# Kernel tuning notes

Hardware: AMD Instinct MI355X
Metric: run time of the kernel (lower is better)

The kernel has to match this reference:

```python
import jax, jax.numpy as jnp
import numpy as np

N_NODES = 50000
N_EDGES = 800000
IN_DIM = 128
E_FEATS = 64
H = 8
D = IN_DIM // H
NEG_SLOPE = 0.2


def setup_inputs() -> dict:
    key = jax.random.key(0)
    ks = jax.random.split(key, 9)
    h = jax.random.normal(ks[0], (N_NODES, IN_DIM), dtype=jnp.float32)
    edge_features = jax.random.normal(ks[1], (N_EDGES, E_FEATS), dtype=jnp.float32)
    src = jax.random.randint(ks[2], (N_EDGES,), 0, N_NODES, dtype=jnp.int32)
    dst = jax.random.randint(ks[3], (N_EDGES,), 0, N_NODES, dtype=jnp.int32)
    s = 0.05
    Wq = jax.random.normal(ks[4], (IN_DIM, IN_DIM), dtype=jnp.float32) * s
    Wk = jax.random.normal(ks[5], (IN_DIM, IN_DIM), dtype=jnp.float32) * s
    Wv = jax.random.normal(ks[6], (IN_DIM, IN_DIM), dtype=jnp.float32) * s
    We = jax.random.normal(ks[7], (H, E_FEATS), dtype=jnp.float32) * s
    Wres = jax.random.normal(ks[8], (IN_DIM, IN_DIM), dtype=jnp.float32) * s
    return {"h": h, "edge_features": edge_features, "src": src, "dst": dst,
            "Wq": Wq, "Wk": Wk, "Wv": Wv, "We": We, "Wres": Wres}


def reference(h, edge_features, src, dst, Wq, Wk, Wv, We, Wres):
    N = h.shape[0]
    # QKV projections (feat_drop is identity at eval)
    q = (h @ Wq.T).reshape(N, H, D)
    k = (h @ Wk.T).reshape(N, H, D)
    v = (h @ Wv.T).reshape(N, H, D)
    # ee / m_att are computed in the original forward but never used (dead code)
    _ee = edge_features @ We.T  # [E, H]

    # v_dot_u('q','k'): dot(q[dst], k[src]) per edge, per head -> [E, H]
    e = jnp.einsum('ehd,ehd->eh', q[dst], k[src])
    e = jnp.where(e >= 0, e, NEG_SLOPE * e)  # leaky_relu

    # edge_softmax over incoming edges of each destination node
    m = jax.ops.segment_max(e, dst, num_segments=N)          # [N, H]
    ex = jnp.exp(e - m[dst])                                 # [E, H]
    z = jax.ops.segment_sum(ex, dst, num_segments=N)         # [N, H]
    alpha = ex / z[dst]                                      # [E, H] (attn_drop identity)

    # weighted aggregation: sum_e alpha * v[src]
    msg = v[src] * alpha[:, :, None]                         # [E, H, D]
    rst = jax.ops.segment_sum(msg, dst, num_segments=N)      # [N, H, D]
    rst = rst.reshape(N, H * D)
    rst = rst + h @ Wres.T                                   # residual
    return rst
```

## Files before the change

### kernel.cpp

```cpp
#include <hip/hip_runtime.h>


#define NEG_SLOPE 0.2f
#define CB 1024

typedef __attribute__((ext_vector_type(8))) short short8;
typedef __attribute__((ext_vector_type(4))) float f32x4;

__device__ __forceinline__ unsigned short f2bf(float f) {
    unsigned int u = __builtin_bit_cast(unsigned int, f);
    u = (u + 0x7fffu + ((u >> 16) & 1u)) >> 16;
    return (unsigned short)u;
}
__device__ __forceinline__ float bf2f(unsigned short s) {
    unsigned int u = (unsigned int)s << 16;
    return __builtin_bit_cast(float, u);
}

__global__ __launch_bounds__(256) void zero_wconv_kernel(
    const float* __restrict__ Wq, const float* __restrict__ Wk,
    const float* __restrict__ Wv, const float* __restrict__ Wres,
    unsigned short* __restrict__ wpk, int* __restrict__ cnt,
    int* __restrict__ csr_pad, int n4)
{
    int t = blockIdx.x * 256 + threadIdx.x;
    if (t < 8192) {
        int l = t & 63;
        int v = t >> 6;
        int kk = v & 3;
        int wct = v >> 2;
        int ct = wct & 7;
        int w = wct >> 3;
        const float* W = (w == 0) ? Wq : (w == 1) ? Wk : (w == 2) ? Wv : Wres;
        const float* srcp = W + (size_t)(ct * 16 + (l & 15)) * 128 + kk * 32 + (l >> 4) * 8;
        float4 lo = *reinterpret_cast<const float4*>(srcp);
        float4 hi = *reinterpret_cast<const float4*>(srcp + 4);
        short8 o;
        o[0] = (short)f2bf(lo.x); o[1] = (short)f2bf(lo.y);
        o[2] = (short)f2bf(lo.z); o[3] = (short)f2bf(lo.w);
        o[4] = (short)f2bf(hi.x); o[5] = (short)f2bf(hi.y);
        o[6] = (short)f2bf(hi.z); o[7] = (short)f2bf(hi.w);
        *reinterpret_cast<short8*>(wpk + (size_t)t * 8) = o;
        if (t < 64) csr_pad[t] = 0;
    } else {
        int u = t - 8192;
        if (u < n4) reinterpret_cast<int4*>(cnt)[u] = make_int4(0, 0, 0, 0);
    }
}

__global__ __launch_bounds__(256) void proj_count_kernel(
    const float* __restrict__ h,
    const unsigned short* __restrict__ wpk,
    unsigned short* __restrict__ qb, unsigned char* __restrict__ kvb,
    float* __restrict__ kvscl, unsigned short* __restrict__ resb,
    const int* __restrict__ dst, int* __restrict__ cnt,
    int N, int E, int PB)
{
    if (blockIdx.x >= PB) {
        int start = (blockIdx.x - PB) * 256 + threadIdx.x;
        for (int e = start; e < E; e += CB * 256)
            atomicAdd(&cnt[dst[e]], 1);
        return;
    }

    const int wid = threadIdx.x >> 6;
    const int lane = threadIdx.x & 63;
    const int row0 = blockIdx.x * 128 + wid * 32;
    const int r = lane & 15, g = lane >> 4;

    short8 afrag[2][4];
    #pragma unroll
    for (int grp = 0; grp < 2; ++grp) {
        int arow = row0 + grp * 16 + r;
        if (arow >= N) arow = N - 1;
        const float* hrow = h + (size_t)arow * 128 + g * 8;
        #pragma unroll
        for (int kk = 0; kk < 4; ++kk) {
            float4 lo = *reinterpret_cast<const float4*>(hrow + kk * 32);
            float4 hi = *reinterpret_cast<const float4*>(hrow + kk * 32 + 4);
            short8 a;
            a[0] = (short)f2bf(lo.x); a[1] = (short)f2bf(lo.y);
            a[2] = (short)f2bf(lo.z); a[3] = (short)f2bf(lo.w);
            a[4] = (short)f2bf(hi.x); a[5] = (short)f2bf(hi.y);
            a[6] = (short)f2bf(hi.z); a[7] = (short)f2bf(hi.w);
            afrag[grp][kk] = a;
        }
    }

    #pragma unroll
    for (int sec = 0; sec < 2; ++sec) {
        const int w = (sec == 0) ? 0 : 3;
        unsigned short* O = (sec == 0) ? qb : resb;
        #pragma unroll
        for (int ct = 0; ct < 8; ++ct) {
            const unsigned short* bp =
                wpk + ((size_t)((w * 8 + ct) * 4) * 64 + lane) * 8;
            f32x4 acc[2];
            acc[0] = (f32x4)(0.f); acc[1] = (f32x4)(0.f);
            #pragma unroll
            for (int kk = 0; kk < 4; ++kk) {
                short8 bfrag = *reinterpret_cast<const short8*>(bp + (size_t)kk * 512);
                acc[0] = __builtin_amdgcn_mfma_f32_16x16x32_bf16(
                    afrag[0][kk], bfrag, acc[0], 0, 0, 0);
                acc[1] = __builtin_amdgcn_mfma_f32_16x16x32_bf16(
                    afrag[1][kk], bfrag, acc[1], 0, 0, 0);
            }
            #pragma unroll
            for (int grp = 0; grp < 2; ++grp)
                #pragma unroll
                for (int j = 0; j < 4; ++j) {
                    int orow = row0 + grp * 16 + g * 4 + j;
                    if (orow < N)
                        O[(size_t)orow * 128 + ct * 16 + r] = f2bf(acc[grp][j]);
                }
        }
    }

    #pragma unroll
    for (int sec = 0; sec < 2; ++sec) {
        const int w = 1 + sec;
        f32x4 av[2][8];
        #pragma unroll
        for (int grp = 0; grp < 2; ++grp)
            #pragma unroll
            for (int ct = 0; ct < 8; ++ct) av[grp][ct] = (f32x4)(0.f);

        #pragma unroll
        for (int ct = 0; ct < 8; ++ct) {
            const unsigned short* bp =
                wpk + ((size_t)((w * 8 + ct) * 4) * 64 + lane) * 8;
            #pragma unroll
            for (int kk = 0; kk < 4; ++kk) {
                short8 bfrag = *reinterpret_cast<const short8*>(bp + (size_t)kk * 512);
                av[0][ct] = __builtin_amdgcn_mfma_f32_16x16x32_bf16(
                    afrag[0][kk], bfrag, av[0][ct], 0, 0, 0);
                av[1][ct] = __builtin_amdgcn_mfma_f32_16x16x32_bf16(
                    afrag[1][kk], bfrag, av[1][ct], 0, 0, 0);
            }
        }

        #pragma unroll
        for (int grp = 0; grp < 2; ++grp)
            #pragma unroll
            for (int j = 0; j < 4; ++j) {
                int orow = row0 + grp * 16 + g * 4 + j;
                float m = fabsf(av[grp][0][j]);
                #pragma unroll
                for (int ct = 1; ct < 8; ++ct)
                    m = fmaxf(m, fabsf(av[grp][ct][j]));
                #pragma unroll
                for (int s = 1; s < 16; s <<= 1)
                    m = fmaxf(m, __shfl_xor(m, s, 64));
                float scale = m * (1.f / 127.f);
                float inv = (m > 0.f) ? 127.f / m : 0.f;
                if (orow < N) {
                    #pragma unroll
                    for (int ct = 0; ct < 8; ++ct) {
                        int qv = (int)rintf(av[grp][ct][j] * inv);
                        kvb[(size_t)orow * 256 + 32 * ct + 8 * (r >> 2)
                            + (r & 3) + sec * 4] = (unsigned char)(signed char)qv;
                    }
                    if (r == 0) kvscl[2 * orow + sec] = scale;
                }
            }
    }
}

__global__ __launch_bounds__(256) void blocksum_kernel(
    const int* __restrict__ cnt, int* __restrict__ bsum, int N)
{
    __shared__ int ws[4];
    const int tid = threadIdx.x;
    int base = blockIdx.x * 1024 + tid * 4;
    int s = 0;
    if (base + 3 < N) {
        int4 v = *reinterpret_cast<const int4*>(cnt + base);
        s = v.x + v.y + v.z + v.w;
    } else {
        for (int i = 0; i < 4; ++i)
            if (base + i < N) s += cnt[base + i];
    }
    #pragma unroll
    for (int m = 32; m >= 1; m >>= 1) s += __shfl_xor(s, m, 64);
    if ((tid & 63) == 0) ws[tid >> 6] = s;
    __syncthreads();
    if (tid == 0) bsum[blockIdx.x] = ws[0] + ws[1] + ws[2] + ws[3];
}

__global__ __launch_bounds__(256) void scanfinal_kernel(
    const int* __restrict__ cnt, const int* __restrict__ bsum,
    int* __restrict__ row_start, int* __restrict__ cursor,
    int N, int E, int NB)
{
    __shared__ int sboff;
    __shared__ int wsum[4];
    const int tid = threadIdx.x, lane = tid & 63, w = tid >> 6;

    if (tid < 64) {
        int v = (tid < NB && tid < blockIdx.x) ? bsum[tid] : 0;
        #pragma unroll
        for (int m = 32; m >= 1; m >>= 1) v += __shfl_xor(v, m, 64);
        if (tid == 0) sboff = v;
    }
    __syncthreads();

    int base = blockIdx.x * 1024 + tid * 4;
    int a0 = 0, a1 = 0, a2 = 0, a3 = 0;
    if (base + 3 < N) {
        int4 v = *reinterpret_cast<const int4*>(cnt + base);
        a0 = v.x; a1 = v.y; a2 = v.z; a3 = v.w;
    } else {
        if (base + 0 < N) a0 = cnt[base + 0];
        if (base + 1 < N) a1 = cnt[base + 1];
        if (base + 2 < N) a2 = cnt[base + 2];
        if (base + 3 < N) a3 = cnt[base + 3];
    }
    const int tsum = a0 + a1 + a2 + a3;
    int v = tsum;
    #pragma unroll
    for (int off = 1; off < 64; off <<= 1) {
        int t = __shfl_up(v, off, 64);
        if (lane >= off) v += t;
    }
    if (lane == 63) wsum[w] = v;
    __syncthreads();
    int woff = 0;
    for (int i = 0; i < w; ++i) woff += wsum[i];
    int run = sboff + woff + v - tsum;

    int r0 = run, r1 = run + a0, r2 = r1 + a1, r3 = r2 + a2;
    if (base + 3 < N) {
        int4 o = make_int4(r0, r1, r2, r3);
        *reinterpret_cast<int4*>(row_start + base) = o;
        *reinterpret_cast<int4*>(cursor + base) = o;
    } else {
        int rr[4] = {r0, r1, r2, r3};
        for (int i = 0; i < 4; ++i)
            if (base + i < N) { row_start[base + i] = rr[i]; cursor[base + i] = rr[i]; }
    }
    if (blockIdx.x == 0 && tid == 0) row_start[N] = E;
}

__global__ __launch_bounds__(256) void scatter_kernel(
    const int* __restrict__ src, const int* __restrict__ dst,
    int* __restrict__ cursor, int* __restrict__ csr_src, int E)
{
    int e = blockIdx.x * 256 + threadIdx.x;
    if (e < E) {
        int d = dst[e];
        int pos = atomicAdd(&cursor[d], 1);
        csr_src[pos] = src[e];
    }
}

__global__ __launch_bounds__(256) void fused_agg_kernel(
    const unsigned short* __restrict__ qb,
    const unsigned char* __restrict__ kvb,
    const float2* __restrict__ kvscl,
    const unsigned short* __restrict__ resb,
    const int* __restrict__ row_start, const int* __restrict__ csr_src,
    float* __restrict__ rst, int N)
{
    const int lane = threadIdx.x & 63;
    const int j = lane & 31;
    const int half = lane >> 5;
    const int node = blockIdx.x * 4 + (threadIdx.x >> 6);
    if (node >= N) return;

    const int beg = row_start[node];
    const int nE  = row_start[node + 1] - beg;
    const int* cp = csr_src + beg;

    ushort4 qraw = *reinterpret_cast<const ushort4*>(qb + (size_t)node * 128 + 4 * j);
    const float q0 = bf2f(qraw.x), q1 = bf2f(qraw.y),
                q2 = bf2f(qraw.z), q3 = bf2f(qraw.w);

    float zA = 0.f, zB = 0.f;
    float aA0 = 0.f, aA1 = 0.f, aA2 = 0.f, aA3 = 0.f;
    float aB0 = 0.f, aB1 = 0.f, aB2 = 0.f, aB3 = 0.f;

    if (nE > 0) {
        int sa = cp[half];
        int sb = cp[half + 2];

        for (int i = 0; i < nE; i += 4) {
            const int ii = i + half;
            const float m0 = (ii < nE) ? 1.f : 0.f;
            const float m1 = (ii + 2 < nE) ? 1.f : 0.f;
            const int s0 = sa, s1 = sb;
            sa = cp[ii + 4];
            sb = cp[ii + 6];

            uint2 kv0 = *reinterpret_cast<const uint2*>(kvb + (size_t)s0 * 256 + 8 * j);
            uint2 kv1 = *reinterpret_cast<const uint2*>(kvb + (size_t)s1 * 256 + 8 * j);
            float2 sc0 = kvscl[s0];
            float2 sc1 = kvscl[s1];

            float p0 = q0 * (float)(signed char)(kv0.x)
                     + q1 * (float)(signed char)(kv0.x >> 8)
                     + q2 * (float)(signed char)(kv0.x >> 16)
                     + q3 * (float)(signed char)(kv0.x >> 24);
            float p1 = q0 * (float)(signed char)(kv1.x)
                     + q1 * (float)(signed char)(kv1.x >> 8)
                     + q2 * (float)(signed char)(kv1.x >> 16)
                     + q3 * (float)(signed char)(kv1.x >> 24);
            p0 += __shfl_xor(p0, 1, 64);
            p0 += __shfl_xor(p0, 2, 64);
            p1 += __shfl_xor(p1, 1, 64);
            p1 += __shfl_xor(p1, 2, 64);
            p0 *= sc0.x;
            p1 *= sc1.x;
            float e0 = (p0 >= 0.f) ? p0 : NEG_SLOPE * p0;
            float e1 = (p1 >= 0.f) ? p1 : NEG_SLOPE * p1;
            e0 = m0 * __expf(e0);
            e1 = m1 * __expf(e1);
            zA += e0;
            zB += e1;
            const float f0 = e0 * sc0.y;
            const float f1 = e1 * sc1.y;
            aA0 = fmaf(f0, (float)(signed char)(kv0.y),       aA0);
            aA1 = fmaf(f0, (float)(signed char)(kv0.y >> 8),  aA1);
            aA2 = fmaf(f0, (float)(signed char)(kv0.y >> 16), aA2);
            aA3 = fmaf(f0, (float)(signed char)(kv0.y >> 24), aA3);
            aB0 = fmaf(f1, (float)(signed char)(kv1.y),       aB0);
            aB1 = fmaf(f1, (float)(signed char)(kv1.y >> 8),  aB1);
            aB2 = fmaf(f1, (float)(signed char)(kv1.y >> 16), aB2);
            aB3 = fmaf(f1, (float)(signed char)(kv1.y >> 24), aB3);
        }
    }

    float a0 = aA0 + aB0, a1 = aA1 + aB1, a2 = aA2 + aB2, a3 = aA3 + aB3;
    float z = zA + zB;
    a0 += __shfl_xor(a0, 32, 64);
    a1 += __shfl_xor(a1, 32, 64);
    a2 += __shfl_xor(a2, 32, 64);
    a3 += __shfl_xor(a3, 32, 64);
    z  += __shfl_xor(z, 32, 64);

    if (half == 0) {
        const size_t base = (size_t)node * 128 + 4 * j;
        ushort4 rb = *reinterpret_cast<const ushort4*>(resb + base);
        float inv = (nE > 0) ? 1.f / z : 0.f;
        float4 rv;
        rv.x = fmaf(a0, inv, bf2f(rb.x));
        rv.y = fmaf(a1, inv, bf2f(rb.y));
        rv.z = fmaf(a2, inv, bf2f(rb.z));
        rv.w = fmaf(a3, inv, bf2f(rb.w));
        *reinterpret_cast<float4*>(rst + base) = rv;
    }
}

extern "C" void kernel_launch(void* const* d_in, const int* in_sizes, int n_in,
                              void* d_out, int out_size, void* d_ws, size_t ws_size,
                              hipStream_t stream) {
    const float* h    = (const float*)d_in[0];
    const int*   src  = (const int*)d_in[2];
    const int*   dst  = (const int*)d_in[3];
    const float* Wq   = (const float*)d_in[4];
    const float* Wk   = (const float*)d_in[5];
    const float* Wv   = (const float*)d_in[6];
    const float* Wres = (const float*)d_in[8];
    float* rst = (float*)d_out;

    const int N = in_sizes[0] / 128;
    const int E = in_sizes[2];

    unsigned short* qb   = (unsigned short*)d_ws;
    unsigned short* resb = qb + (size_t)N * 128;
    unsigned char*  kvb  = (unsigned char*)(resb + (size_t)N * 128);
    float*          kvscl = (float*)(kvb + (size_t)N * 256);
    unsigned short* wpk  = (unsigned short*)(kvscl + 2 * N);
    int* cnt       = (int*)(wpk + 4 * 16384);
    int* row_start = cnt + N;
    int* cursor    = row_start + (N + 1);
    int* csr_src   = cursor + N;
    int* bsum      = csr_src + E + 64;

    const int n4 = N / 4;
    const int NB = (N + 1023) / 1024;
    const int PB = (N + 127) / 128;

    zero_wconv_kernel<<<(8192 + n4 + 255) / 256, 256, 0, stream>>>(
        Wq, Wk, Wv, Wres, wpk, cnt, csr_src + E, n4);
    proj_count_kernel<<<PB + CB, 256, 0, stream>>>(
        h, wpk, qb, kvb, kvscl, resb, dst, cnt, N, E, PB);
    blocksum_kernel<<<NB, 256, 0, stream>>>(cnt, bsum, N);
    scanfinal_kernel<<<NB, 256, 0, stream>>>(cnt, bsum, row_start, cursor,
                                             N, E, NB);
    scatter_kernel<<<(E + 255) / 256, 256, 0, stream>>>(src, dst, cursor,
                                                        csr_src, E);
    fused_agg_kernel<<<(N + 3) / 4, 256, 0, stream>>>(
        qb, kvb, (const float2*)kvscl, resb, row_start, csr_src, rst, N);
}
```

Baseline: 159.0 us.

## Recompute K/V projections in two passes and store scales as bf16

The K/V quantization stops keeping all 16 accumulator tiles live. It runs the MFMAs once to compute per-row abs max, then recomputes them to quantize, which reduces register pressure at the cost of doubled K/V matmul work. The per-node dequantization scales are stored as packed bf16 pairs, halving the scale gather in the aggregation kernel. This costs slightly lower scale precision.

```diff
diff --git a/kernel.cpp b/kernel.cpp
--- a/kernel.cpp
+++ b/kernel.cpp
@@ -52,7 +52,7 @@
     const float* __restrict__ h,
     const unsigned short* __restrict__ wpk,
     unsigned short* __restrict__ qb, unsigned char* __restrict__ kvb,
-    float* __restrict__ kvscl, unsigned short* __restrict__ resb,
+    unsigned short* __restrict__ kvscl16, unsigned short* __restrict__ resb,
     const int* __restrict__ dst, int* __restrict__ cnt,
     int N, int E, int PB)
 {
@@ -119,50 +119,75 @@
     #pragma unroll
     for (int sec = 0; sec < 2; ++sec) {
         const int w = 1 + sec;
-        f32x4 av[2][8];
+
+        float mx[2][4];
         #pragma unroll
         for (int grp = 0; grp < 2; ++grp)
             #pragma unroll
-            for (int ct = 0; ct < 8; ++ct) av[grp][ct] = (f32x4)(0.f);
+            for (int j = 0; j < 4; ++j) mx[grp][j] = 0.f;
 
         #pragma unroll
         for (int ct = 0; ct < 8; ++ct) {
             const unsigned short* bp =
                 wpk + ((size_t)((w * 8 + ct) * 4) * 64 + lane) * 8;
+            f32x4 acc[2];
+            acc[0] = (f32x4)(0.f); acc[1] = (f32x4)(0.f);
             #pragma unroll
             for (int kk = 0; kk < 4; ++kk) {
                 short8 bfrag = *reinterpret_cast<const short8*>(bp + (size_t)kk * 512);
-                av[0][ct] = __builtin_amdgcn_mfma_f32_16x16x32_bf16(
-                    afrag[0][kk], bfrag, av[0][ct], 0, 0, 0);
-                av[1][ct] = __builtin_amdgcn_mfma_f32_16x16x32_bf16(
-                    afrag[1][kk], bfrag, av[1][ct], 0, 0, 0);
+                acc[0] = __builtin_amdgcn_mfma_f32_16x16x32_bf16(
+                    afrag[0][kk], bfrag, acc[0], 0, 0, 0);
+                acc[1] = __builtin_amdgcn_mfma_f32_16x16x32_bf16(
+                    afrag[1][kk], bfrag, acc[1], 0, 0, 0);
             }
+            #pragma unroll
+            for (int grp = 0; grp < 2; ++grp)
+                #pragma unroll
+                for (int j = 0; j < 4; ++j)
+                    mx[grp][j] = fmaxf(mx[grp][j], fabsf(acc[grp][j]));
         }
 
+        float inv[2][4];
         #pragma unroll
         for (int grp = 0; grp < 2; ++grp)
             #pragma unroll
             for (int j = 0; j < 4; ++j) {
-                int orow = row0 + grp * 16 + g * 4 + j;
-                float m = fabsf(av[grp][0][j]);
-                #pragma unroll
-                for (int ct = 1; ct < 8; ++ct)
-                    m = fmaxf(m, fabsf(av[grp][ct][j]));
+                float m = mx[grp][j];
                 #pragma unroll
                 for (int s = 1; s < 16; s <<= 1)
                     m = fmaxf(m, __shfl_xor(m, s, 64));
-                float scale = m * (1.f / 127.f);
-                float inv = (m > 0.f) ? 127.f / m : 0.f;
-                if (orow < N) {
-                    #pragma unroll
-                    for (int ct = 0; ct < 8; ++ct) {
-                        int qv = (int)rintf(av[grp][ct][j] * inv);
+                inv[grp][j] = (m > 0.f) ? 127.f / m : 0.f;
+                int orow = row0 + grp * 16 + g * 4 + j;
+                if (orow < N && r == 0)
+                    kvscl16[2 * orow + sec] = f2bf(m * (1.f / 127.f));
+            }
+
+        #pragma unroll
+        for (int ct = 0; ct < 8; ++ct) {
+            const unsigned short* bp =
+                wpk + ((size_t)((w * 8 + ct) * 4) * 64 + lane) * 8;
+            f32x4 acc[2];
+            acc[0] = (f32x4)(0.f); acc[1] = (f32x4)(0.f);
+            #pragma unroll
+            for (int kk = 0; kk < 4; ++kk) {
+                short8 bfrag = *reinterpret_cast<const short8*>(bp + (size_t)kk * 512);
+                acc[0] = __builtin_amdgcn_mfma_f32_16x16x32_bf16(
+                    afrag[0][kk], bfrag, acc[0], 0, 0, 0);
+                acc[1] = __builtin_amdgcn_mfma_f32_16x16x32_bf16(
+                    afrag[1][kk], bfrag, acc[1], 0, 0, 0);
+            }
+            #pragma unroll
+            for (int grp = 0; grp < 2; ++grp)
+                #pragma unroll
+                for (int j = 0; j < 4; ++j) {
+                    int orow = row0 + grp * 16 + g * 4 + j;
+                    if (orow < N) {
+                        int qv = (int)rintf(acc[grp][j] * inv[grp][j]);
                         kvb[(size_t)orow * 256 + 32 * ct + 8 * (r >> 2)
                             + (r & 3) + sec * 4] = (unsigned char)(signed char)qv;
                     }
-                    if (r == 0) kvscl[2 * orow + sec] = scale;
                 }
-            }
+        }
     }
 }
 
@@ -256,7 +281,7 @@
 __global__ __launch_bounds__(256) void fused_agg_kernel(
     const unsigned short* __restrict__ qb,
     const unsigned char* __restrict__ kvb,
-    const float2* __restrict__ kvscl,
+    const unsigned int* __restrict__ kvscl32,
     const unsigned short* __restrict__ resb,
     const int* __restrict__ row_start, const int* __restrict__ csr_src,
     float* __restrict__ rst, int N)
@@ -293,8 +318,8 @@
 
             uint2 kv0 = *reinterpret_cast<const uint2*>(kvb + (size_t)s0 * 256 + 8 * j);
             uint2 kv1 = *reinterpret_cast<const uint2*>(kvb + (size_t)s1 * 256 + 8 * j);
-            float2 sc0 = kvscl[s0];
-            float2 sc1 = kvscl[s1];
+            unsigned int sw0 = kvscl32[s0];
+            unsigned int sw1 = kvscl32[s1];
 
             float p0 = q0 * (float)(signed char)(kv0.x)
                      + q1 * (float)(signed char)(kv0.x >> 8)
@@ -308,16 +333,16 @@
             p0 += __shfl_xor(p0, 2, 64);
             p1 += __shfl_xor(p1, 1, 64);
             p1 += __shfl_xor(p1, 2, 64);
-            p0 *= sc0.x;
-            p1 *= sc1.x;
+            p0 *= bf2f((unsigned short)(sw0 & 0xffff));
+            p1 *= bf2f((unsigned short)(sw1 & 0xffff));
             float e0 = (p0 >= 0.f) ? p0 : NEG_SLOPE * p0;
             float e1 = (p1 >= 0.f) ? p1 : NEG_SLOPE * p1;
             e0 = m0 * __expf(e0);
             e1 = m1 * __expf(e1);
             zA += e0;
             zB += e1;
-            const float f0 = e0 * sc0.y;
-            const float f1 = e1 * sc1.y;
+            const float f0 = e0 * bf2f((unsigned short)(sw0 >> 16));
+            const float f1 = e1 * bf2f((unsigned short)(sw1 >> 16));
             aA0 = fmaf(f0, (float)(signed char)(kv0.y),       aA0);
             aA1 = fmaf(f0, (float)(signed char)(kv0.y >> 8),  aA1);
             aA2 = fmaf(f0, (float)(signed char)(kv0.y >> 16), aA2);
@@ -365,11 +390,11 @@
     const int N = in_sizes[0] / 128;
     const int E = in_sizes[2];
 
-    unsigned short* qb   = (unsigned short*)d_ws;
-    unsigned short* resb = qb + (size_t)N * 128;
-    unsigned char*  kvb  = (unsigned char*)(resb + (size_t)N * 128);
-    float*          kvscl = (float*)(kvb + (size_t)N * 256);
-    unsigned short* wpk  = (unsigned short*)(kvscl + 2 * N);
+    unsigned short* qb    = (unsigned short*)d_ws;
+    unsigned short* resb  = qb + (size_t)N * 128;
+    unsigned char*  kvb   = (unsigned char*)(resb + (size_t)N * 128);
+    unsigned short* kvscl = (unsigned short*)(kvb + (size_t)N * 256);
+    unsigned short* wpk   = kvscl + 2 * N;
     int* cnt       = (int*)(wpk + 4 * 16384);
     int* row_start = cnt + N;
     int* cursor    = row_start + (N + 1);
@@ -390,5 +415,6 @@
     scatter_kernel<<<(E + 255) / 256, 256, 0, stream>>>(src, dst, cursor,
                                                         csr_src, E);
     fused_agg_kernel<<<(N + 3) / 4, 256, 0, stream>>>(
-        qb, kvb, (const float2*)kvscl, resb, row_start, csr_src, rst, N);
-}
+        qb, kvb, (const unsigned int*)kvscl, resb, row_start, csr_src,
+        rst, N);
+}
```

Result: no change. 159.5 us (+0.3%).
